# Kernel optimization log

Hardware: AMD Instinct MI355X
Metric: run time of the kernel (lower is better)

## Reference

```python
import jax, jax.numpy as jnp
import numpy as np

D_MODEL = 1024
NUM_HEADS = 16


def setup_inputs() -> dict:
    key = jax.random.key(0)
    ks = jax.random.split(key, 5)
    std = float(np.sqrt(2.0 / (D_MODEL + D_MODEL)))
    def w(k):
        # approximate trunc_normal init with clipped normal (init only; math of fwd unaffected)
        v = jax.random.truncated_normal(k, -3.0, 3.0, (D_MODEL, D_MODEL), jnp.float32) * std
        return v
    x = jax.random.normal(ks[0], (4, 2048, D_MODEL), jnp.float32)
    return {
        "x": x,
        "wq": w(ks[1]),
        "wk": w(ks[2]),
        "wv": w(ks[3]),
        "wo": w(ks[4]),
    }


def reference(x, wq, wk, wv, wo):
    b, s, d = x.shape
    h = NUM_HEADS
    dk = d // h
    # Linear: einsum('o i, ... i -> ... o')
    def proj(w):
        y = jnp.einsum('oi,bsi->bso', w, x)
        return y.reshape(b, s, h, dk).transpose(0, 2, 1, 3)  # b h s dk
    Q, K, V = proj(wq), proj(wk), proj(wv)
    scale = 1.0 / jnp.sqrt(jnp.asarray(dk, x.dtype))
    scores = jnp.einsum('bhqd,bhkd->bhqk', Q, K) * scale
    mask = jnp.tril(jnp.ones((s, s), dtype=bool))
    scores = jnp.where(mask, scores, -jnp.inf)
    attn = jax.nn.softmax(scores, axis=-1)
    out = jnp.einsum('bhqk,bhkd->bhqd', attn, V)
    out = out.transpose(0, 2, 1, 3).reshape(b, s, d)
    return jnp.einsum('oi,bsi->bso', wo, out)
```

## Files before the change

### kernel.cpp

```cpp
#include <hip/hip_runtime.h>
#include <hip/hip_bf16.h>


typedef __bf16 bf16x8 __attribute__((ext_vector_type(8)));
typedef __bf16 bf16x4 __attribute__((ext_vector_type(4)));
typedef float  f32x4  __attribute__((ext_vector_type(4)));
typedef float  f32x16 __attribute__((ext_vector_type(16)));
typedef unsigned int u32x4_t __attribute__((ext_vector_type(4)));

#define GLOBAL_AS __attribute__((address_space(1)))
#define LDS_AS    __attribute__((address_space(3)))

__device__ __forceinline__ void gload16(const void* g, void* l) {
    __builtin_amdgcn_global_load_lds((const GLOBAL_AS void*)g, (LDS_AS void*)l, 16, 0, 0);
}

__device__ __forceinline__ unsigned int cvtpk_bf16(float lo, float hi) {
    unsigned int r;
    asm("v_cvt_pk_bf16_f32 %0, %1, %2" : "=v"(r) : "v"(lo), "v"(hi));
    return r;
}

#define WAITVM8 asm volatile("s_waitcnt vmcnt(8)" ::: "memory")
#define WAITVM0 asm volatile("s_waitcnt vmcnt(0)" ::: "memory")
#define SCHEDB  __builtin_amdgcn_sched_barrier(0)

__global__ __launch_bounds__(256) void cast_kernel(
    const float* __restrict__ x, const float* __restrict__ wq,
    const float* __restrict__ wk, const float* __restrict__ wv,
    const float* __restrict__ wo, __bf16* __restrict__ xb, __bf16* __restrict__ wb) {
    int bid = blockIdx.x;
    const float* src; __bf16* dst; int base;
    if (bid < 4096) {
        src = x; dst = xb; base = bid * 2048;
    } else {
        int r = bid - 4096; int wi = r >> 9;
        src = (wi == 0) ? wq : (wi == 1) ? wk : (wi == 2) ? wv : wo;
        dst = wb + wi * 1048576; base = (r & 511) * 2048;
    }
    int idx = base + threadIdx.x * 8;
    float4 a = *(const float4*)(src + idx);
    float4 b = *(const float4*)(src + idx + 4);
    bf16x8 o;
    o[0] = (__bf16)a.x; o[1] = (__bf16)a.y; o[2] = (__bf16)a.z; o[3] = (__bf16)a.w;
    o[4] = (__bf16)b.x; o[5] = (__bf16)b.y; o[6] = (__bf16)b.z; o[7] = (__bf16)b.w;
    *(bf16x8*)(dst + idx) = o;
}

__global__ __launch_bounds__(256) void gemm_qkv_kernel(
    const __bf16* __restrict__ A, const __bf16* __restrict__ W,
    __bf16* __restrict__ Qb, __bf16* __restrict__ Kb, __bf16* __restrict__ Vt,
    float qscale) {
    __shared__ __align__(16) char lds[65536];
    const int t = threadIdx.x;
    const int wid = t >> 6, lane = t & 63;
    const int g = lane >> 4, m = lane & 15;
    const int wm = wid >> 1, wn = wid & 1;
    const int bid = (blockIdx.x & 7) * 192 + (blockIdx.x >> 3);
    const int mt = bid / 24, nt = bid % 24;
    const int m0 = mt * 128, n0 = nt * 128;
    const bool isV = (n0 >= 2048);

    const __bf16* sA[4]; const __bf16* sB[4]; int dA[4];
#pragma unroll
    for (int i = 0; i < 4; ++i) {
        const int ci = i * 256 + t;
        const int row = ci >> 3;
        const int k8 = (ci & 7) ^ (row & 7);
        sA[i] = A + (size_t)(m0 + row) * 1024 + k8 * 8;
        sB[i] = W + (size_t)(n0 + row) * 1024 + k8 * 8;
        dA[i] = ci * 16;
    }
    auto stage = [&](int kt, char* buf) {
#pragma unroll
        for (int i = 0; i < 4; ++i) gload16(sA[i] + kt * 64, buf + dA[i]);
#pragma unroll
        for (int i = 0; i < 4; ++i) gload16(sB[i] + kt * 64, buf + 16384 + dA[i]);
    };

    const int sw = (m & 7) << 4;
    const int offA = (wm * 64 + m) * 128 + ((g << 4) ^ sw);
    const int offB = (wn * 64 + m) * 128 + ((g << 4) ^ sw);

    stage(0, lds);

    f32x4 acc[4][4] = {};
    for (int kt = 0; kt < 16; ++kt) {
        char* cbuf = lds + (kt & 1) * 32768;
        if (kt < 15) {
            stage(kt + 1, lds + ((kt + 1) & 1) * 32768);
            WAITVM8;
        } else {
            WAITVM0;
        }
        SCHEDB;
        __builtin_amdgcn_s_barrier();
        SCHEDB;
        const char* bA = cbuf;
        const char* bB = cbuf + 16384;
        bf16x8 a0[4], b0[4], a1[4], b1[4];
#pragma unroll
        for (int i = 0; i < 4; ++i) {
            a0[i] = *(const bf16x8*)(bA + (offA + i * 2048));
            b0[i] = *(const bf16x8*)(bB + (offB + i * 2048));
            a1[i] = *(const bf16x8*)(bA + ((offA + i * 2048) ^ 64));
            b1[i] = *(const bf16x8*)(bB + ((offB + i * 2048) ^ 64));
        }
        __builtin_amdgcn_s_setprio(1);
        if (isV) {
#pragma unroll
            for (int mi = 0; mi < 4; ++mi)
#pragma unroll
                for (int ni = 0; ni < 4; ++ni)
                    acc[mi][ni] = __builtin_amdgcn_mfma_f32_16x16x32_bf16(a0[mi], b0[ni], acc[mi][ni], 0, 0, 0);
#pragma unroll
            for (int mi = 0; mi < 4; ++mi)
#pragma unroll
                for (int ni = 0; ni < 4; ++ni)
                    acc[mi][ni] = __builtin_amdgcn_mfma_f32_16x16x32_bf16(a1[mi], b1[ni], acc[mi][ni], 0, 0, 0);
        } else {
#pragma unroll
            for (int mi = 0; mi < 4; ++mi)
#pragma unroll
                for (int ni = 0; ni < 4; ++ni)
                    acc[mi][ni] = __builtin_amdgcn_mfma_f32_16x16x32_bf16(b0[ni], a0[mi], acc[mi][ni], 0, 0, 0);
#pragma unroll
            for (int mi = 0; mi < 4; ++mi)
#pragma unroll
                for (int ni = 0; ni < 4; ++ni)
                    acc[mi][ni] = __builtin_amdgcn_mfma_f32_16x16x32_bf16(b1[ni], a1[mi], acc[mi][ni], 0, 0, 0);
        }
        __builtin_amdgcn_s_setprio(0);
        if (kt < 15) {
            SCHEDB;
            __builtin_amdgcn_s_barrier();
            SCHEDB;
        }
    }

    if (isV) {
        const int bb = m0 >> 11;
        const int sb = (m0 & 2047) + wm * 64 + 4 * g;
        const int hbase = ((n0 - 2048) >> 6) + wn;
#pragma unroll
        for (int mi = 0; mi < 4; ++mi)
#pragma unroll
            for (int ni = 0; ni < 4; ++ni) {
                const int d = ni * 16 + m;
                bf16x4 pk;
                pk[0] = (__bf16)(acc[mi][ni][0]); pk[1] = (__bf16)(acc[mi][ni][1]);
                pk[2] = (__bf16)(acc[mi][ni][2]); pk[3] = (__bf16)(acc[mi][ni][3]);
                *(bf16x4*)(Vt + ((size_t)(bb * 16 + hbase) * 64 + d) * 2048 + sb + mi * 16) = pk;
            }
    } else {
        __bf16* C = (n0 < 1024) ? Qb : Kb;
        const float sc = (n0 < 1024) ? qscale : 1.f;
        const int cb = (n0 & 1023) + wn * 64 + 4 * g;
        const int row = m0 + wm * 64 + m;
#pragma unroll
        for (int mi = 0; mi < 4; ++mi)
#pragma unroll
            for (int ni = 0; ni < 4; ++ni) {
                bf16x4 pk;
                pk[0] = (__bf16)(acc[mi][ni][0] * sc); pk[1] = (__bf16)(acc[mi][ni][1] * sc);
                pk[2] = (__bf16)(acc[mi][ni][2] * sc); pk[3] = (__bf16)(acc[mi][ni][3] * sc);
                *(bf16x4*)(C + (size_t)(row + mi * 16) * 1024 + cb + ni * 16) = pk;
            }
    }
}

__global__ __launch_bounds__(256) void gemm_out_kernel(
    const __bf16* __restrict__ A, const __bf16* __restrict__ W, float* __restrict__ out) {
    __shared__ __align__(16) char lds[65536];
    const int t = threadIdx.x;
    const int wid = t >> 6, lane = t & 63;
    const int g = lane >> 4, m = lane & 15;
    const int wm = wid >> 1, wn = wid & 1;
    const int bid = (blockIdx.x & 7) * 64 + (blockIdx.x >> 3);
    const int mt = bid >> 3, nt = bid & 7;
    const int m0 = mt * 128, n0 = nt * 128;

    const __bf16* sA[4]; const __bf16* sB[4]; int dA[4];
#pragma unroll
    for (int i = 0; i < 4; ++i) {
        const int ci = i * 256 + t;
        const int row = ci >> 3;
        const int k8 = (ci & 7) ^ (row & 7);
        sA[i] = A + (size_t)(m0 + row) * 1024 + k8 * 8;
        sB[i] = W + (size_t)(n0 + row) * 1024 + k8 * 8;
        dA[i] = ci * 16;
    }
    auto stage = [&](int kt, char* buf) {
#pragma unroll
        for (int i = 0; i < 4; ++i) gload16(sA[i] + kt * 64, buf + dA[i]);
#pragma unroll
        for (int i = 0; i < 4; ++i) gload16(sB[i] + kt * 64, buf + 16384 + dA[i]);
    };

    const int sw = (m & 7) << 4;
    const int offA = (wm * 64 + m) * 128 + ((g << 4) ^ sw);
    const int offB = (wn * 64 + m) * 128 + ((g << 4) ^ sw);

    stage(0, lds);

    f32x4 acc[4][4] = {};
    for (int kt = 0; kt < 16; ++kt) {
        char* cbuf = lds + (kt & 1) * 32768;
        if (kt < 15) {
            stage(kt + 1, lds + ((kt + 1) & 1) * 32768);
            WAITVM8;
        } else {
            WAITVM0;
        }
        SCHEDB;
        __builtin_amdgcn_s_barrier();
        SCHEDB;
        const char* bA = cbuf;
        const char* bB = cbuf + 16384;
        bf16x8 a0[4], b0[4], a1[4], b1[4];
#pragma unroll
        for (int i = 0; i < 4; ++i) {
            a0[i] = *(const bf16x8*)(bA + (offA + i * 2048));
            b0[i] = *(const bf16x8*)(bB + (offB + i * 2048));
            a1[i] = *(const bf16x8*)(bA + ((offA + i * 2048) ^ 64));
            b1[i] = *(const bf16x8*)(bB + ((offB + i * 2048) ^ 64));
        }
        __builtin_amdgcn_s_setprio(1);
#pragma unroll
        for (int mi = 0; mi < 4; ++mi)
#pragma unroll
            for (int ni = 0; ni < 4; ++ni)
                acc[mi][ni] = __builtin_amdgcn_mfma_f32_16x16x32_bf16(b0[ni], a0[mi], acc[mi][ni], 0, 0, 0);
#pragma unroll
        for (int mi = 0; mi < 4; ++mi)
#pragma unroll
            for (int ni = 0; ni < 4; ++ni)
                acc[mi][ni] = __builtin_amdgcn_mfma_f32_16x16x32_bf16(b1[ni], a1[mi], acc[mi][ni], 0, 0, 0);
        __builtin_amdgcn_s_setprio(0);
        if (kt < 15) {
            SCHEDB;
            __builtin_amdgcn_s_barrier();
            SCHEDB;
        }
    }

    const int row = m0 + wm * 64 + m;
    const int col = n0 + wn * 64 + 4 * g;
#pragma unroll
    for (int mi = 0; mi < 4; ++mi)
#pragma unroll
        for (int ni = 0; ni < 4; ++ni)
            *(f32x4*)(out + (size_t)(row + mi * 16) * 1024 + col + ni * 16) = acc[mi][ni];
}

__global__ __launch_bounds__(128, 2) void attn_kernel(
    const __bf16* __restrict__ Qb, const __bf16* __restrict__ Kb,
    const __bf16* __restrict__ Vt, __bf16* __restrict__ Ob) {
    __shared__ __align__(16) char lds[32768];
    const int t = threadIdx.x;
    const int w = t >> 6, lane = t & 63;
    const int l31 = lane & 31, hi = lane >> 5;
    const int qb = (blockIdx.x >> 3) & 15;
    const int bh = (blockIdx.x & 7) | ((blockIdx.x >> 7) << 3);
    const size_t sbase = (size_t)(bh >> 4) * 2048;
    const int hoff = (bh & 15) * 64;

    const char* Kbase = (const char*)Kb + (sbase * 1024 + hoff) * 2;
    const char* Vbase = (const char*)Vt + (size_t)bh * 262144;
    const int srow = lane >> 3;
    const int scol = ((lane & 7) ^ srow) << 4;
    const int sw = (l31 & 7) << 4;
    int colx[4];
#pragma unroll
    for (int i = 0; i < 4; ++i) colx[i] = (32 * i + 16 * hi) ^ sw;

    auto stage = [&](int kv0, char* lK) {
        char* lV = lK + 8192;
#pragma unroll
        for (int i = 0; i < 4; ++i) {
            const int chunk = i * 2 + w;
            const int row = chunk * 8 + srow;
            gload16(Kbase + (size_t)(kv0 + row) * 2048 + scol, lK + chunk * 1024);
            gload16(Vbase + (size_t)row * 4096 + (size_t)kv0 * 2 + scol, lV + chunk * 1024);
        }
    };

    const int q0A = qb * 64 + w * 32;
    const int q0B = (31 - qb) * 64 + w * 32;
    const int qA = q0A + l31, qB = q0B + l31;
    const int nstream = 32 - qb;

    const __bf16* qrowA = Qb + (sbase + q0A + l31) * 1024 + hoff + 8 * hi;
    const __bf16* qrowB = Qb + (sbase + q0B + l31) * 1024 + hoff + 8 * hi;
    bf16x8 qfA[4], qfB[4];
#pragma unroll
    for (int cq = 0; cq < 4; ++cq) {
        qfA[cq] = *(const bf16x8*)(qrowA + 16 * cq);
        qfB[cq] = *(const bf16x8*)(qrowB + 16 * cq);
    }

    f32x16 oA0 = {}, oA1 = {}, oB0 = {}, oB1 = {};
    float mA = -__builtin_inff(), lA = 0.f;
    float mB = -__builtin_inff(), lB = 0.f;

    auto process = [&](const f32x16& s0r, const f32x16& s1r, int qq, bool diag,
                       int kv0, float& mrun, float& lrun, f32x16& o0, f32x16& o1,
                       const char* lV) {
        float pp[32];
#pragma unroll
        for (int rr = 0; rr < 16; ++rr) { pp[rr] = s0r[rr]; pp[16 + rr] = s1r[rr]; }
        if (diag) {
#pragma unroll
            for (int rr = 0; rr < 16; ++rr) {
                const int kvl = (rr & 3) + 8 * (rr >> 2) + 4 * hi;
                if (kv0 + kvl > qq)      pp[rr]      = -__builtin_inff();
                if (kv0 + 32 + kvl > qq) pp[16 + rr] = -__builtin_inff();
            }
        }
        float m8[8];
#pragma unroll
        for (int i = 0; i < 8; ++i)
            m8[i] = fmaxf(fmaxf(pp[4 * i], pp[4 * i + 1]), fmaxf(pp[4 * i + 2], pp[4 * i + 3]));
        float tmax = fmaxf(fmaxf(fmaxf(m8[0], m8[1]), fmaxf(m8[2], m8[3])),
                           fmaxf(fmaxf(m8[4], m8[5]), fmaxf(m8[6], m8[7])));
        const bool skip = __all(tmax <= mrun + 8.f);
        if (!skip) {
            float tq = fmaxf(tmax, __shfl_xor(tmax, 32));
            float mnew = fmaxf(mrun, tq);
            float al = __builtin_amdgcn_exp2f(mrun - mnew);
            lrun *= al;
#pragma unroll
            for (int rr = 0; rr < 16; ++rr) { o0[rr] *= al; o1[rr] *= al; }
            mrun = mnew;
        }
#pragma unroll
        for (int rr = 0; rr < 32; ++rr) pp[rr] = __builtin_amdgcn_exp2f(pp[rr] - mrun);
        float s8[8];
#pragma unroll
        for (int i = 0; i < 8; ++i)
            s8[i] = (pp[4 * i] + pp[4 * i + 1]) + (pp[4 * i + 2] + pp[4 * i + 3]);
        float rsum = ((s8[0] + s8[1]) + (s8[2] + s8[3])) + ((s8[4] + s8[5]) + (s8[6] + s8[7]));
        rsum += __shfl_xor(rsum, 32);
        lrun += rsum;

        __builtin_amdgcn_s_setprio(1);
#pragma unroll
        for (int cc = 0; cc < 4; ++cc) {
            const int pb = cc * 8;
            unsigned int A0 = cvtpk_bf16(pp[pb + 0], pp[pb + 1]);
            unsigned int A1 = cvtpk_bf16(pp[pb + 2], pp[pb + 3]);
            unsigned int B0 = cvtpk_bf16(pp[pb + 4], pp[pb + 5]);
            unsigned int B1 = cvtpk_bf16(pp[pb + 6], pp[pb + 7]);
            asm("v_permlane32_swap_b32 %0, %1" : "+v"(A0), "+v"(B0));
            asm("v_permlane32_swap_b32 %0, %1" : "+v"(A1), "+v"(B1));
            u32x4_t wvv; wvv[0] = A0; wvv[1] = A1; wvv[2] = B0; wvv[3] = B1;
            bf16x8 pa = __builtin_bit_cast(bf16x8, wvv);
            const int vcol = (32 * cc + 16 * hi) ^ sw;
            bf16x8 v0 = *(const bf16x8*)(lV + l31 * 128 + vcol);
            bf16x8 v1 = *(const bf16x8*)(lV + (l31 + 32) * 128 + vcol);
            o0 = __builtin_amdgcn_mfma_f32_32x32x16_bf16(v0, pa, o0, 0, 0, 0);
            o1 = __builtin_amdgcn_mfma_f32_32x32x16_bf16(v1, pa, o1, 0, 0, 0);
        }
        __builtin_amdgcn_s_setprio(0);
    };

    stage(0, lds);

    for (int tt = 0; tt < nstream; ++tt) {
        const int cur = tt & 1;
        char* lcur = lds + cur * 16384;
        __builtin_amdgcn_s_barrier();
        if (tt + 1 < nstream) {
            stage((tt + 1) * 64, lds + (cur ^ 1) * 16384);
            WAITVM8;
        } else {
            WAITVM0;
        }
        __builtin_amdgcn_s_barrier();
        __builtin_amdgcn_sched_barrier(0);

        const int kv0 = tt * 64;
        const char* lK = lcur;
        const char* lV = lcur + 8192;
        const bool dual = (tt <= qb);

        f32x16 sA0 = {}, sA1 = {}, sB0 = {}, sB1 = {};
        __builtin_amdgcn_s_setprio(1);
        if (dual) {
#pragma unroll
            for (int cc = 0; cc < 4; ++cc) {
                bf16x8 k0 = *(const bf16x8*)(lK + l31 * 128 + colx[cc]);
                bf16x8 k1 = *(const bf16x8*)(lK + (l31 + 32) * 128 + colx[cc]);
                sA0 = __builtin_amdgcn_mfma_f32_32x32x16_bf16(k0, qfA[cc], sA0, 0, 0, 0);
                sA1 = __builtin_amdgcn_mfma_f32_32x32x16_bf16(k1, qfA[cc], sA1, 0, 0, 0);
                sB0 = __builtin_amdgcn_mfma_f32_32x32x16_bf16(k0, qfB[cc], sB0, 0, 0, 0);
                sB1 = __builtin_amdgcn_mfma_f32_32x32x16_bf16(k1, qfB[cc], sB1, 0, 0, 0);
            }
        } else {
#pragma unroll
            for (int cc = 0; cc < 4; ++cc) {
                bf16x8 k0 = *(const bf16x8*)(lK + l31 * 128 + colx[cc]);
                bf16x8 k1 = *(const bf16x8*)(lK + (l31 + 32) * 128 + colx[cc]);
                sB0 = __builtin_amdgcn_mfma_f32_32x32x16_bf16(k0, qfB[cc], sB0, 0, 0, 0);
                sB1 = __builtin_amdgcn_mfma_f32_32x32x16_bf16(k1, qfB[cc], sB1, 0, 0, 0);
            }
        }
        __builtin_amdgcn_s_setprio(0);

        if (dual)
            process(sA0, sA1, qA, tt == qb, kv0, mA, lA, oA0, oA1, lV);
        process(sB0, sB1, qB, tt == nstream - 1, kv0, mB, lB, oB0, oB1, lV);
    }

    {
        const float inv = 1.f / lA;
        __bf16* orow = Ob + (sbase + q0A + l31) * 1024 + hoff;
#pragma unroll
        for (int rq = 0; rq < 4; ++rq) {
            bf16x4 e0, e1;
#pragma unroll
            for (int jj = 0; jj < 4; ++jj) {
                e0[jj] = (__bf16)(oA0[rq * 4 + jj] * inv);
                e1[jj] = (__bf16)(oA1[rq * 4 + jj] * inv);
            }
            *(bf16x4*)(orow + 4 * hi + 8 * rq) = e0;
            *(bf16x4*)(orow + 32 + 4 * hi + 8 * rq) = e1;
        }
    }
    {
        const float inv = 1.f / lB;
        __bf16* orow = Ob + (sbase + q0B + l31) * 1024 + hoff;
#pragma unroll
        for (int rq = 0; rq < 4; ++rq) {
            bf16x4 e0, e1;
#pragma unroll
            for (int jj = 0; jj < 4; ++jj) {
                e0[jj] = (__bf16)(oB0[rq * 4 + jj] * inv);
                e1[jj] = (__bf16)(oB1[rq * 4 + jj] * inv);
            }
            *(bf16x4*)(orow + 4 * hi + 8 * rq) = e0;
            *(bf16x4*)(orow + 32 + 4 * hi + 8 * rq) = e1;
        }
    }
}

extern "C" void kernel_launch(void* const* d_in, const int* in_sizes, int n_in,
                              void* d_out, int out_size, void* d_ws, size_t ws_size,
                              hipStream_t stream) {
    const float* x  = (const float*)d_in[0];
    const float* wq = (const float*)d_in[1];
    const float* wk = (const float*)d_in[2];
    const float* wv = (const float*)d_in[3];
    const float* wo = (const float*)d_in[4];

    char* ws = (char*)d_ws;
    __bf16* xb = (__bf16*)(ws);
    __bf16* wb = (__bf16*)(ws + 16777216);
    __bf16* Qb = (__bf16*)(ws + 25165824);
    __bf16* Kb = (__bf16*)(ws + 41943040);
    __bf16* Vt = (__bf16*)(ws + 58720256);
    __bf16* Ob = (__bf16*)(ws + 75497472);

    const float qscale = 0.18033688011112043f;

    cast_kernel<<<6144, 256, 0, stream>>>(x, wq, wk, wv, wo, xb, wb);
    gemm_qkv_kernel<<<1536, 256, 0, stream>>>(xb, wb, Qb, Kb, Vt, qscale);
    attn_kernel<<<1024, 128, 0, stream>>>(Qb, Kb, Vt, Ob);
    gemm_out_kernel<<<512, 256, 0, stream>>>(Ob, wb + 3145728, (float*)d_out);
}
```

Measured before the change: 174.1 us.

## Split paired causal query strips across four waves per attention block

The attention block grows from 2 waves, each handling both the early and late query strip, to 4 waves with each wave owning one 32-row slice of one strip. K/V staging is split across four waves, so each issues half the loads and the wait count drops accordingly. Waves on the short strip skip compute once past their diagonal but keep joining the barriers. This doubles the waves that can overlap MFMA and softmax and cuts per-wave register pressure, but the early-strip waves sit idle for much of the loop.

Measured after the change: 208.2 us. 19.6% more time.

```diff
diff --git a/kernel.cpp b/kernel.cpp
--- a/kernel.cpp
+++ b/kernel.cpp
@@ -22,6 +22,7 @@
 }
 
 #define WAITVM8 asm volatile("s_waitcnt vmcnt(8)" ::: "memory")
+#define WAITVM4 asm volatile("s_waitcnt vmcnt(4)" ::: "memory")
 #define WAITVM0 asm volatile("s_waitcnt vmcnt(0)" ::: "memory")
 #define SCHEDB  __builtin_amdgcn_sched_barrier(0)
 
@@ -253,15 +254,16 @@
             *(f32x4*)(out + (size_t)(row + mi * 16) * 1024 + col + ni * 16) = acc[mi][ni];
 }
 
-__global__ __launch_bounds__(128, 2) void attn_kernel(
+__global__ __launch_bounds__(256) void attn_kernel(
     const __bf16* __restrict__ Qb, const __bf16* __restrict__ Kb,
     const __bf16* __restrict__ Vt, __bf16* __restrict__ Ob) {
     __shared__ __align__(16) char lds[32768];
     const int t = threadIdx.x;
     const int w = t >> 6, lane = t & 63;
     const int l31 = lane & 31, hi = lane >> 5;
-    const int qb = (blockIdx.x >> 3) & 15;
-    const int bh = (blockIdx.x & 7) | ((blockIdx.x >> 7) << 3);
+    const int x = blockIdx.x;
+    const int qb = (x >> 3) & 15;
+    const int bh = (x & 7) | ((x >> 7) << 3);
     const size_t sbase = (size_t)(bh >> 4) * 2048;
     const int hoff = (bh & 15) * 64;
 
@@ -274,47 +276,72 @@
 #pragma unroll
     for (int i = 0; i < 4; ++i) colx[i] = (32 * i + 16 * hi) ^ sw;
 
+    const int strip = (w < 2) ? qb : (31 - qb);
+    const int q0w = strip * 64 + (w & 1) * 32;
+    const int q = q0w + l31;
+    const int myt = strip + 1;
+    const int nstream = 32 - qb;
+
     auto stage = [&](int kv0, char* lK) {
         char* lV = lK + 8192;
 #pragma unroll
-        for (int i = 0; i < 4; ++i) {
-            const int chunk = i * 2 + w;
+        for (int i = 0; i < 2; ++i) {
+            const int chunk = i * 4 + w;
             const int row = chunk * 8 + srow;
             gload16(Kbase + (size_t)(kv0 + row) * 2048 + scol, lK + chunk * 1024);
             gload16(Vbase + (size_t)row * 4096 + (size_t)kv0 * 2 + scol, lV + chunk * 1024);
         }
     };
 
-    const int q0A = qb * 64 + w * 32;
-    const int q0B = (31 - qb) * 64 + w * 32;
-    const int qA = q0A + l31, qB = q0B + l31;
-    const int nstream = 32 - qb;
-
-    const __bf16* qrowA = Qb + (sbase + q0A + l31) * 1024 + hoff + 8 * hi;
-    const __bf16* qrowB = Qb + (sbase + q0B + l31) * 1024 + hoff + 8 * hi;
-    bf16x8 qfA[4], qfB[4];
-#pragma unroll
-    for (int cq = 0; cq < 4; ++cq) {
-        qfA[cq] = *(const bf16x8*)(qrowA + 16 * cq);
-        qfB[cq] = *(const bf16x8*)(qrowB + 16 * cq);
-    }
-
-    f32x16 oA0 = {}, oA1 = {}, oB0 = {}, oB1 = {};
-    float mA = -__builtin_inff(), lA = 0.f;
-    float mB = -__builtin_inff(), lB = 0.f;
-
-    auto process = [&](const f32x16& s0r, const f32x16& s1r, int qq, bool diag,
-                       int kv0, float& mrun, float& lrun, f32x16& o0, f32x16& o1,
-                       const char* lV) {
+    const __bf16* qrow = Qb + (sbase + q0w + l31) * 1024 + hoff + 8 * hi;
+    bf16x8 qf[4];
+#pragma unroll
+    for (int cq = 0; cq < 4; ++cq) qf[cq] = *(const bf16x8*)(qrow + 16 * cq);
+
+    f32x16 o0 = {}, o1 = {};
+    float mrun = -__builtin_inff(), lrun = 0.f;
+
+    stage(0, lds);
+
+    for (int tt = 0; tt < nstream; ++tt) {
+        const int cur = tt & 1;
+        char* lcur = lds + cur * 16384;
+        __builtin_amdgcn_s_barrier();
+        if (tt + 1 < nstream) {
+            stage((tt + 1) * 64, lds + (cur ^ 1) * 16384);
+            WAITVM4;
+        } else {
+            WAITVM0;
+        }
+        __builtin_amdgcn_s_barrier();
+        __builtin_amdgcn_sched_barrier(0);
+
+        if (tt >= myt) continue;
+
+        const int kv0 = tt * 64;
+        const char* lK = lcur;
+        const char* lV = lcur + 8192;
+
+        f32x16 s0 = {}, s1 = {};
+        __builtin_amdgcn_s_setprio(1);
+#pragma unroll
+        for (int cc = 0; cc < 4; ++cc) {
+            bf16x8 k0 = *(const bf16x8*)(lK + l31 * 128 + colx[cc]);
+            bf16x8 k1 = *(const bf16x8*)(lK + (l31 + 32) * 128 + colx[cc]);
+            s0 = __builtin_amdgcn_mfma_f32_32x32x16_bf16(k0, qf[cc], s0, 0, 0, 0);
+            s1 = __builtin_amdgcn_mfma_f32_32x32x16_bf16(k1, qf[cc], s1, 0, 0, 0);
+        }
+        __builtin_amdgcn_s_setprio(0);
+
         float pp[32];
 #pragma unroll
-        for (int rr = 0; rr < 16; ++rr) { pp[rr] = s0r[rr]; pp[16 + rr] = s1r[rr]; }
-        if (diag) {
+        for (int rr = 0; rr < 16; ++rr) { pp[rr] = s0[rr]; pp[16 + rr] = s1[rr]; }
+        if (tt == strip) {
 #pragma unroll
             for (int rr = 0; rr < 16; ++rr) {
                 const int kvl = (rr & 3) + 8 * (rr >> 2) + 4 * hi;
-                if (kv0 + kvl > qq)      pp[rr]      = -__builtin_inff();
-                if (kv0 + 32 + kvl > qq) pp[16 + rr] = -__builtin_inff();
+                if (kv0 + kvl > q)      pp[rr]      = -__builtin_inff();
+                if (kv0 + 32 + kvl > q) pp[16 + rr] = -__builtin_inff();
             }
         }
         float m8[8];
@@ -362,85 +389,20 @@
             o1 = __builtin_amdgcn_mfma_f32_32x32x16_bf16(v1, pa, o1, 0, 0, 0);
         }
         __builtin_amdgcn_s_setprio(0);
-    };
-
-    stage(0, lds);
-
-    for (int tt = 0; tt < nstream; ++tt) {
-        const int cur = tt & 1;
-        char* lcur = lds + cur * 16384;
-        __builtin_amdgcn_s_barrier();
-        if (tt + 1 < nstream) {
-            stage((tt + 1) * 64, lds + (cur ^ 1) * 16384);
-            WAITVM8;
-        } else {
-            WAITVM0;
-        }
-        __builtin_amdgcn_s_barrier();
-        __builtin_amdgcn_sched_barrier(0);
-
-        const int kv0 = tt * 64;
-        const char* lK = lcur;
-        const char* lV = lcur + 8192;
-        const bool dual = (tt <= qb);
-
-        f32x16 sA0 = {}, sA1 = {}, sB0 = {}, sB1 = {};
-        __builtin_amdgcn_s_setprio(1);
-        if (dual) {
-#pragma unroll
-            for (int cc = 0; cc < 4; ++cc) {
-                bf16x8 k0 = *(const bf16x8*)(lK + l31 * 128 + colx[cc]);
-                bf16x8 k1 = *(const bf16x8*)(lK + (l31 + 32) * 128 + colx[cc]);
-                sA0 = __builtin_amdgcn_mfma_f32_32x32x16_bf16(k0, qfA[cc], sA0, 0, 0, 0);
-                sA1 = __builtin_amdgcn_mfma_f32_32x32x16_bf16(k1, qfA[cc], sA1, 0, 0, 0);
-                sB0 = __builtin_amdgcn_mfma_f32_32x32x16_bf16(k0, qfB[cc], sB0, 0, 0, 0);
-                sB1 = __builtin_amdgcn_mfma_f32_32x32x16_bf16(k1, qfB[cc], sB1, 0, 0, 0);
-            }
-        } else {
-#pragma unroll
-            for (int cc = 0; cc < 4; ++cc) {
-                bf16x8 k0 = *(const bf16x8*)(lK + l31 * 128 + colx[cc]);
-                bf16x8 k1 = *(const bf16x8*)(lK + (l31 + 32) * 128 + colx[cc]);
-                sB0 = __builtin_amdgcn_mfma_f32_32x32x16_bf16(k0, qfB[cc], sB0, 0, 0, 0);
-                sB1 = __builtin_amdgcn_mfma_f32_32x32x16_bf16(k1, qfB[cc], sB1, 0, 0, 0);
-            }
-        }
-        __builtin_amdgcn_s_setprio(0);
-
-        if (dual)
-            process(sA0, sA1, qA, tt == qb, kv0, mA, lA, oA0, oA1, lV);
-        process(sB0, sB1, qB, tt == nstream - 1, kv0, mB, lB, oB0, oB1, lV);
-    }
-
-    {
-        const float inv = 1.f / lA;
-        __bf16* orow = Ob + (sbase + q0A + l31) * 1024 + hoff;
-#pragma unroll
-        for (int rq = 0; rq < 4; ++rq) {
-            bf16x4 e0, e1;
-#pragma unroll
-            for (int jj = 0; jj < 4; ++jj) {
-                e0[jj] = (__bf16)(oA0[rq * 4 + jj] * inv);
-                e1[jj] = (__bf16)(oA1[rq * 4 + jj] * inv);
-            }
-            *(bf16x4*)(orow + 4 * hi + 8 * rq) = e0;
-            *(bf16x4*)(orow + 32 + 4 * hi + 8 * rq) = e1;
-        }
-    }
-    {
-        const float inv = 1.f / lB;
-        __bf16* orow = Ob + (sbase + q0B + l31) * 1024 + hoff;
-#pragma unroll
-        for (int rq = 0; rq < 4; ++rq) {
-            bf16x4 e0, e1;
-#pragma unroll
-            for (int jj = 0; jj < 4; ++jj) {
-                e0[jj] = (__bf16)(oB0[rq * 4 + jj] * inv);
-                e1[jj] = (__bf16)(oB1[rq * 4 + jj] * inv);
-            }
-            *(bf16x4*)(orow + 4 * hi + 8 * rq) = e0;
-            *(bf16x4*)(orow + 32 + 4 * hi + 8 * rq) = e1;
-        }
+    }
+
+    const float inv = 1.f / lrun;
+    __bf16* orow = Ob + (sbase + q0w + l31) * 1024 + hoff;
+#pragma unroll
+    for (int rq = 0; rq < 4; ++rq) {
+        bf16x4 e0, e1;
+#pragma unroll
+        for (int jj = 0; jj < 4; ++jj) {
+            e0[jj] = (__bf16)(o0[rq * 4 + jj] * inv);
+            e1[jj] = (__bf16)(o1[rq * 4 + jj] * inv);
+        }
+        *(bf16x4*)(orow + 4 * hi + 8 * rq) = e0;
+        *(bf16x4*)(orow + 32 + 4 * hi + 8 * rq) = e1;
     }
 }
 
@@ -465,6 +427,6 @@
 
     cast_kernel<<<6144, 256, 0, stream>>>(x, wq, wk, wv, wo, xb, wb);
     gemm_qkv_kernel<<<1536, 256, 0, stream>>>(xb, wb, Qb, Kb, Vt, qscale);
-    attn_kernel<<<1024, 128, 0, stream>>>(Qb, Kb, Vt, Ob);
+    attn_kernel<<<1024, 256, 0, stream>>>(Qb, Kb, Vt, Ob);
     gemm_out_kernel<<<512, 256, 0, stream>>>(Ob, wb + 3145728, (float*)d_out);
 }
```
